# Kernel optimization log

Hardware: AMD Instinct MI355X
Metric: run time of the kernel (lower is better)

The kernel has to match this reference:

```python
import jax, jax.numpy as jnp
import numpy as np

B, L, HID, TRANS = 16384, 512, 768, 128


def setup_inputs() -> dict:
    key = jax.random.key(0)
    ks = jax.random.split(key, 12)
    def lin(k, out_d, in_d):
        kw, kb = jax.random.split(k)
        s = 1.0 / np.sqrt(in_d)
        return (jax.random.uniform(kw, (out_d, in_d), jnp.float32, -s, s),
                jax.random.uniform(kb, (out_d,), jnp.float32, -s, s))
    W_text, b_text = lin(ks[0], TRANS, HID)
    W_label, b_label = lin(ks[1], TRANS, HID)
    W0, b0 = lin(ks[2], TRANS, 2 * TRANS)
    W1, b1 = lin(ks[3], TRANS, TRANS)
    W2, b2 = lin(ks[4], 1, TRANS)
    target = jax.random.randint(ks[5], (B, L), 0, 2, jnp.int32)
    # guarantee every sample has at least one positive label (torch.mean on empty would NaN)
    target = target.at[:, 0].set(1)
    return {
        "text_embed": jax.random.normal(ks[6], (B, HID), jnp.float32),
        "label_embed": jax.random.normal(ks[7], (L, HID), jnp.float32),
        "target": target,
        "perm": jax.random.permutation(ks[8], B).astype(jnp.int32),
        "W_text": W_text, "b_text": b_text,
        "W_label": W_label, "b_label": b_label,
        "W0": W0, "b0": b0, "W1": W1, "b1": b1, "W2": W2, "b2": b2,
    }


def _network(t, l, W_text, b_text, W_label, b_label, W0, b0, W1, b1, W2, b2):
    tt = t @ W_text.T + b_text            # [B, trans]
    ll = l @ W_label.T + b_label          # [B, trans]
    h = jnp.concatenate([tt, ll], axis=1)  # [B, 2*trans]
    h = jax.nn.relu(h @ W0.T + b0)
    h = jax.nn.relu(h @ W1.T + b1)
    return h @ W2.T + b2                  # [B, 1]


def reference(text_embed, label_embed, target, perm,
              W_text, b_text, W_label, b_label, W0, b0, W1, b1, W2, b2):
    # variable-length mean pooling of label embeddings selected by the multi-hot target
    mask = target.astype(text_embed.dtype)                 # [B, L]
    counts = jnp.maximum(mask.sum(axis=1, keepdims=True), 1.0)
    label_feature_y = (mask @ label_embed) / counts        # [B, hid]
    negative_text = text_embed[perm]                       # shuffled negatives
    params = (W_text, b_text, W_label, b_label, W0, b0, W1, b1, W2, b2)
    E_joint = -jnp.mean(jax.nn.softplus(-_network(text_embed, label_feature_y, *params)))
    E_marginal = jnp.mean(jax.nn.softplus(_network(negative_text, label_feature_y, *params)))
    return E_marginal - E_joint
```

## Files before the change

### kernel.cpp

```cpp
#include <hip/hip_runtime.h>
#include <math.h>

#define BATCH 16384
#define LBL   512
#define HID   768
#define TR    128

typedef unsigned long long u64;
typedef unsigned short ushort_t;
typedef __attribute__((ext_vector_type(8))) short short8;
typedef __attribute__((ext_vector_type(4))) float f32x4;

__device__ __forceinline__ ushort_t f2bf(float f){
  unsigned u = __builtin_bit_cast(unsigned, f);
  u += 0x7FFFu + ((u >> 16) & 1u);
  return (ushort_t)(u >> 16);
}
__device__ __forceinline__ float bf2f(ushort_t h){
  unsigned u = ((unsigned)h) << 16;
  return __builtin_bit_cast(float, u);
}
__device__ __forceinline__ float softplusf(float x){
  return fmaxf(x, 0.0f) + log1pf(expf(-fabsf(x)));
}
__device__ __forceinline__ void gload_lds16(const void* g, void* l){
  __builtin_amdgcn_global_load_lds((const __attribute__((address_space(1))) void*)g,
                                   (__attribute__((address_space(3))) void*)l, 16, 0, 0);
}

__global__ __launch_bounds__(256) void k1(
    const float* __restrict__ W0, const float* __restrict__ Wt, const float* __restrict__ Wl,
    const float* __restrict__ bt, const float* __restrict__ bl, const float* __restrict__ b0,
    const float* __restrict__ W1,
    ushort_t* __restrict__ Msw, ushort_t* __restrict__ Qsw, ushort_t* __restrict__ W1B,
    float* __restrict__ KV, float* __restrict__ out){
  __shared__ float sw[TR];
  int bi = blockIdx.x, t = threadIdx.x;
  if (bi < 256){
    int i = bi & 127;
    int isQ = bi >> 7;
    const float* src = isQ ? Wl : Wt;
    ushort_t* dst = isQ ? Qsw : Msw;
    if (t < TR) sw[t] = W0[(size_t)i*256 + isQ*128 + t];
    if (!isQ && t < 128) W1B[i*128 + t] = f2bf(W1[i*128 + t]);
    __syncthreads();
    int c = t;
    float a0 = 0.f, a1 = 0.f, a2 = 0.f;
    #pragma unroll 8
    for (int a = 0; a < 128; a++){
      float w = sw[a];
      const float* r = src + (size_t)a*HID;
      a0 = fmaf(w, r[c], a0);
      a1 = fmaf(w, r[c+256], a1);
      a2 = fmaf(w, r[c+512], a2);
    }
    int c7 = c & 7;
    dst[(((c      )>>3)<<10) + (i<<3) + c7] = f2bf(a0);
    dst[(((c + 256)>>3)<<10) + (i<<3) + c7] = f2bf(a1);
    dst[(((c + 512)>>3)<<10) + (i<<3) + c7] = f2bf(a2);
  } else {
    if (t < TR){
      float s = b0[t];
      const float* r = W0 + (size_t)t*256;
      for (int a = 0; a < 128; a++) s = fmaf(r[a], bt[a], s);
      for (int a = 0; a < 128; a++) s = fmaf(r[128+a], bl[a], s);
      KV[t] = s;
    }
    if (t == 0) out[0] = 0.f;
  }
}

__device__ __forceinline__ void gemm768_32(const float* ap, const ushort_t* Bsw,
                                           ushort_t* As_, ushort_t* Bs_,
                                           int tid, int wave, int m, int q,
                                           f32x4 acc[2][2]){
  float4 ra0 = *(const float4*)ap;
  float4 ra1 = *(const float4*)(ap + 4);
  {
    const char* gb = (const char*)Bsw;
    char* lb = (char*)Bs_;
    #pragma unroll
    for (int p = 0; p < 4; p++)
      gload_lds16(gb + p*4096 + tid*16, lb + p*4096 + tid*16);
  }
  #pragma unroll
  for (int rt = 0; rt < 2; rt++)
    #pragma unroll
    for (int ct = 0; ct < 2; ct++)
      acc[rt][ct] = (f32x4){0.f,0.f,0.f,0.f};

  for (int c = 0; c < 12; c++){
    int buf = c & 1;
    short8 av;
    av[0] = (short)f2bf(ra0.x); av[1] = (short)f2bf(ra0.y);
    av[2] = (short)f2bf(ra0.z); av[3] = (short)f2bf(ra0.w);
    av[4] = (short)f2bf(ra1.x); av[5] = (short)f2bf(ra1.y);
    av[6] = (short)f2bf(ra1.z); av[7] = (short)f2bf(ra1.w);
    *(short8*)(As_ + (size_t)(buf*32 + (tid >> 3))*80 + (tid & 7)*8) = av;
    __syncthreads();
    if (c < 11){
      ra0 = *(const float4*)(ap + (c+1)*64);
      ra1 = *(const float4*)(ap + (c+1)*64 + 4);
      const char* gb = (const char*)Bsw + (size_t)(c+1)*16384;
      char* lb = (char*)(Bs_ + (buf^1)*8192);
      #pragma unroll
      for (int p = 0; p < 4; p++)
        gload_lds16(gb + p*4096 + tid*16, lb + p*4096 + tid*16);
    }
    #pragma unroll
    for (int kcc = 0; kcc < 2; kcc++){
      short8 bfr[2];
      #pragma unroll
      for (int ct = 0; ct < 2; ct++)
        bfr[ct] = *(const short8*)(Bs_ + buf*8192 + (kcc*4 + q)*1024 + (wave*32 + ct*16 + m)*8);
      #pragma unroll
      for (int rt = 0; rt < 2; rt++){
        short8 a = *(const short8*)(As_ + (size_t)(buf*32 + rt*16 + m)*80 + kcc*32 + q*8);
        #pragma unroll
        for (int ct = 0; ct < 2; ct++)
          acc[rt][ct] = __builtin_amdgcn_mfma_f32_16x16x32_bf16(a, bfr[ct], acc[rt][ct], 0, 0, 0);
      }
    }
  }
}

__global__ __launch_bounds__(256) void k2(
    const float* __restrict__ labe, const ushort_t* __restrict__ Qsw,
    const float* __restrict__ T,    const ushort_t* __restrict__ Msw,
    const float* __restrict__ KV,   const int* __restrict__ tgt,
    ushort_t* __restrict__ Gt, ushort_t* __restrict__ U,
    u64* __restrict__ bits, float* __restrict__ inv){
  __shared__ __align__(16) char uni[43008];
  int bi = blockIdx.x, tid = threadIdx.x;
  int lane = tid & 63, wave = tid >> 6;
  int m = lane & 15, q = lane >> 4;
  int arow = tid >> 3, ak = (tid & 7) * 8;
  ushort_t* Bs_ = (ushort_t*)uni;
  ushort_t* As_ = (ushort_t*)(uni + 32768);

  if (bi < 512){
    int b0r = bi*32;
    #pragma unroll
    for (int rr = 0; rr < 8; rr++){
      int row = b0r + wave*8 + rr;
      const int* rp = tgt + (size_t)row*LBL;
      int v[8];
      #pragma unroll
      for (int c = 0; c < 8; c++) v[c] = rp[c*64 + lane];
      int cnt = 0;
      #pragma unroll
      for (int c = 0; c < 8; c++){
        u64 mm = __ballot(v[c] != 0);
        if (lane == 0){ bits[(size_t)row*8 + c] = mm; cnt += __popcll(mm); }
      }
      if (lane == 0) inv[row] = 1.0f / (float)(cnt < 1 ? 1 : cnt);
    }
  } else if (bi < 528){
    int l0 = (bi - 512) * 32;
    f32x4 accG[2][2];
    gemm768_32(labe + (size_t)(l0 + arow)*HID + ak, Qsw, As_, Bs_, tid, wave, m, q, accG);
    __syncthreads();
    ushort_t (*GTs)[40] = (ushort_t(*)[40])uni;
    #pragma unroll
    for (int rt = 0; rt < 2; rt++)
      #pragma unroll
      for (int ct = 0; ct < 2; ct++){
        int col = wave*32 + ct*16 + m;
        #pragma unroll
        for (int r = 0; r < 4; r++)
          GTs[col][rt*16 + q*4 + r] = f2bf(accG[rt][ct][r]);
      }
    __syncthreads();
    int gi = tid >> 1, half = tid & 1;
    ushort_t* dstp = Gt + (size_t)gi*LBL + l0 + half*16;
    *(short8*)(dstp)     = *(const short8*)&GTs[gi][half*16];
    *(short8*)(dstp + 8) = *(const short8*)&GTs[gi][half*16 + 8];
  } else {
    int r0 = (bi - 528) * 32;
    f32x4 accU[2][2];
    gemm768_32(T + (size_t)(r0 + arow)*HID + ak, Msw, As_, Bs_, tid, wave, m, q, accU);
    #pragma unroll
    for (int rt = 0; rt < 2; rt++)
      #pragma unroll
      for (int ct = 0; ct < 2; ct++){
        int col = wave*32 + ct*16 + m;
        float kv = KV[col];
        #pragma unroll
        for (int r = 0; r < 4; r++)
          U[(size_t)(r0 + rt*16 + q*4 + r)*TR + col] = f2bf(accU[rt][ct][r] + kv);
      }
  }
}

__global__ __launch_bounds__(256) void k3(const ushort_t* __restrict__ U, const ushort_t* __restrict__ Gt,
                                          const u64* __restrict__ BITS_, const float* __restrict__ INV,
                                          const int* __restrict__ perm, const ushort_t* __restrict__ W1b,
                                          const float* __restrict__ b1, const float* __restrict__ W2,
                                          const float* __restrict__ b2, float* __restrict__ out){
  __shared__ __align__(16) u64 bitsS[32*10];
  __shared__ __align__(16) ushort_t h0s[64][136];
  __shared__ float sred[4*4*16*17];
  __shared__ float invs[32];
  __shared__ int   permS[32];

  int tid = threadIdx.x;
  int lane = tid & 63, wave = tid >> 6;
  int m = lane & 15, q = lane >> 4;
  int r0 = blockIdx.x * 32;

  if (tid < 128){
    int row = tid >> 2, seg = tid & 3;
    const int4* src = (const int4*)((const char*)BITS_ + (size_t)(r0+row)*64 + seg*16);
    *(int4*)((char*)bitsS + row*80 + seg*16) = *src;
  } else if (tid < 160){
    invs[tid & 31] = INV[r0 + (tid & 31)];
  } else if (tid < 192){
    permS[tid & 31] = perm[r0 + (tid & 31)];
  }
  __syncthreads();

  float up[2][2][4], un[2][2][4];
  #pragma unroll
  for (int rt = 0; rt < 2; rt++)
    #pragma unroll
    for (int ct = 0; ct < 2; ct++){
      int col = wave*32 + ct*16 + m;
      #pragma unroll
      for (int r = 0; r < 4; r++){
        int rowl = rt*16 + q*4 + r;
        up[rt][ct][r] = bf2f(U[(size_t)(r0 + rowl)*TR + col]);
        un[rt][ct][r] = bf2f(U[(size_t)permS[rowl]*TR + col]);
      }
    }

  const unsigned char* bits_b = (const unsigned char*)bitsS;
  f32x4 accV[2][2] = {{{0,0,0,0},{0,0,0,0}},{{0,0,0,0},{0,0,0,0}}};
  const ushort_t* gp[2];
  #pragma unroll
  for (int ct = 0; ct < 2; ct++)
    gp[ct] = Gt + (size_t)(wave*32 + ct*16 + m)*LBL + q*8;
  short8 bcur[2], bnext[2];
  #pragma unroll
  for (int ct = 0; ct < 2; ct++) bcur[ct] = *(const short8*)(gp[ct]);
  for (int c = 0; c < 16; c++){
    if (c < 15){
      #pragma unroll
      for (int ct = 0; ct < 2; ct++) bnext[ct] = *(const short8*)(gp[ct] + (c+1)*32);
    }
    #pragma unroll
    for (int rt = 0; rt < 2; rt++){
      unsigned bb = bits_b[(rt*16 + m)*80 + c*4 + q];
      short8 a;
      #pragma unroll
      for (int j = 0; j < 8; j++) a[j] = (short)(((bb >> j) & 1u) ? 0x3F80 : 0);
      #pragma unroll
      for (int ct = 0; ct < 2; ct++)
        accV[rt][ct] = __builtin_amdgcn_mfma_f32_16x16x32_bf16(a, bcur[ct], accV[rt][ct], 0, 0, 0);
    }
    #pragma unroll
    for (int ct = 0; ct < 2; ct++) bcur[ct] = bnext[ct];
  }

  #pragma unroll
  for (int rt = 0; rt < 2; rt++)
    #pragma unroll
    for (int ct = 0; ct < 2; ct++){
      int col = wave*32 + ct*16 + m;
      #pragma unroll
      for (int r = 0; r < 4; r++){
        int rowl = rt*16 + q*4 + r;
        float v = accV[rt][ct][r] * invs[rowl];
        h0s[rowl][col]      = f2bf(fmaxf(up[rt][ct][r] + v, 0.f));
        h0s[32 + rowl][col] = f2bf(fmaxf(un[rt][ct][r] + v, 0.f));
      }
    }
  __syncthreads();

  float w2c[2], b1c[2];
  #pragma unroll
  for (int ct = 0; ct < 2; ct++){
    int col = wave*32 + ct*16 + m;
    w2c[ct] = W2[col];
    b1c[ct] = b1[col];
  }
  float b2v = b2[0];

  #pragma unroll
  for (int rt2 = 0; rt2 < 4; rt2++){
    f32x4 accH[2] = {{0,0,0,0},{0,0,0,0}};
    #pragma unroll
    for (int kc = 0; kc < 4; kc++){
      short8 a = *(const short8*)&h0s[rt2*16 + m][kc*32 + q*8];
      #pragma unroll
      for (int ct = 0; ct < 2; ct++){
        short8 b = *(const short8*)(W1b + (size_t)(wave*32 + ct*16 + m)*TR + kc*32 + q*8);
        accH[ct] = __builtin_amdgcn_mfma_f32_16x16x32_bf16(a, b, accH[ct], 0, 0, 0);
      }
    }
    #pragma unroll
    for (int r = 0; r < 4; r++){
      float sp = 0.f;
      #pragma unroll
      for (int ct = 0; ct < 2; ct++)
        sp = fmaf(w2c[ct], fmaxf(accH[ct][r] + b1c[ct], 0.f), sp);
      sred[((wave*4 + rt2)*16 + q*4 + r)*17 + m] = sp;
    }
  }
  __syncthreads();

  if (tid < 64){
    int rt2 = tid >> 4, row = tid & 15;
    float s = b2v;
    #pragma unroll
    for (int wx = 0; wx < 4; wx++)
      #pragma unroll
      for (int n = 0; n < 16; n++) s += sred[((wx*4 + rt2)*16 + row)*17 + n];
    float val = (rt2 < 2) ? softplusf(-s) : softplusf(s);
    #pragma unroll
    for (int off = 32; off > 0; off >>= 1) val += __shfl_down(val, off);
    if (tid == 0) atomicAdd(out, val * (1.0f / (float)BATCH));
  }
}

extern "C" void kernel_launch(void* const* d_in, const int* in_sizes, int n_in,
                              void* d_out, int out_size, void* d_ws, size_t ws_size,
                              hipStream_t stream){
  const float* text = (const float*)d_in[0];
  const float* labe = (const float*)d_in[1];
  const int*   tgt  = (const int*)  d_in[2];
  const int*   perm = (const int*)  d_in[3];
  const float* Wt   = (const float*)d_in[4];
  const float* bt   = (const float*)d_in[5];
  const float* Wl   = (const float*)d_in[6];
  const float* bl   = (const float*)d_in[7];
  const float* W0   = (const float*)d_in[8];
  const float* b0   = (const float*)d_in[9];
  const float* W1   = (const float*)d_in[10];
  const float* b1   = (const float*)d_in[11];
  const float* W2   = (const float*)d_in[12];
  const float* b2   = (const float*)d_in[13];

  char* wsb = (char*)d_ws;
  size_t off = 0;
  auto alloc = [&](size_t bytes){
    size_t r = off;
    off += (bytes + 255) & ~(size_t)255;
    return r;
  };
  ushort_t* MSW = (ushort_t*)(wsb + alloc((size_t)TR*HID*2));
  ushort_t* QSW = (ushort_t*)(wsb + alloc((size_t)TR*HID*2));
  ushort_t* GT  = (ushort_t*)(wsb + alloc((size_t)TR*LBL*2));
  ushort_t* W1B = (ushort_t*)(wsb + alloc((size_t)TR*TR*2));
  float*    KV  = (float*)   (wsb + alloc((size_t)TR*4));
  u64*      BITS= (u64*)     (wsb + alloc((size_t)BATCH*8*8));
  float*    INV = (float*)   (wsb + alloc((size_t)BATCH*4));
  ushort_t* U   = (ushort_t*)(wsb + alloc((size_t)BATCH*TR*2));
  float*    out = (float*)d_out;
  (void)ws_size; (void)in_sizes; (void)n_in; (void)out_size;

  k1<<<257, 256, 0, stream>>>(W0, Wt, Wl, bt, bl, b0, W1, MSW, QSW, W1B, KV, out);
  k2<<<1040, 256, 0, stream>>>(labe, QSW, text, MSW, KV, tgt, GT, U, BITS, INV);
  k3<<<512, 256, 0, stream>>>(U, GT, BITS, INV, perm, W1B, b1, W2, b2, out);
}
```

Before: 175.8 us.

## Fuse text projection GEMM into final kernel, computing permuted negatives directly

The text-side GEMM (T @ Msw + KV) moves out of k2 into k3. Each block computes the projection for its own 32 rows and for the 32 permuted negative rows straight from text_embed, so the bf16 U intermediate and its gather are no longer needed. This removes a global write and read of the U buffer and shrinks k2's grid. The cost is that permuted text rows are projected a second time (double GEMM FLOPs for the text part) and k3 now uses more LDS and registers.

```diff
diff --git a/kernel.cpp b/kernel.cpp
--- a/kernel.cpp
+++ b/kernel.cpp
@@ -15,10 +15,6 @@
   unsigned u = __builtin_bit_cast(unsigned, f);
   u += 0x7FFFu + ((u >> 16) & 1u);
   return (ushort_t)(u >> 16);
-}
-__device__ __forceinline__ float bf2f(ushort_t h){
-  unsigned u = ((unsigned)h) << 16;
-  return __builtin_bit_cast(float, u);
 }
 __device__ __forceinline__ float softplusf(float x){
   return fmaxf(x, 0.0f) + log1pf(expf(-fabsf(x)));
@@ -126,37 +122,18 @@
 
 __global__ __launch_bounds__(256) void k2(
     const float* __restrict__ labe, const ushort_t* __restrict__ Qsw,
-    const float* __restrict__ T,    const ushort_t* __restrict__ Msw,
-    const float* __restrict__ KV,   const int* __restrict__ tgt,
-    ushort_t* __restrict__ Gt, ushort_t* __restrict__ U,
-    u64* __restrict__ bits, float* __restrict__ inv){
+    const int* __restrict__ tgt,
+    ushort_t* __restrict__ Gt, u64* __restrict__ bits, float* __restrict__ inv){
   __shared__ __align__(16) char uni[43008];
   int bi = blockIdx.x, tid = threadIdx.x;
   int lane = tid & 63, wave = tid >> 6;
   int m = lane & 15, q = lane >> 4;
-  int arow = tid >> 3, ak = (tid & 7) * 8;
   ushort_t* Bs_ = (ushort_t*)uni;
   ushort_t* As_ = (ushort_t*)(uni + 32768);
 
-  if (bi < 512){
-    int b0r = bi*32;
-    #pragma unroll
-    for (int rr = 0; rr < 8; rr++){
-      int row = b0r + wave*8 + rr;
-      const int* rp = tgt + (size_t)row*LBL;
-      int v[8];
-      #pragma unroll
-      for (int c = 0; c < 8; c++) v[c] = rp[c*64 + lane];
-      int cnt = 0;
-      #pragma unroll
-      for (int c = 0; c < 8; c++){
-        u64 mm = __ballot(v[c] != 0);
-        if (lane == 0){ bits[(size_t)row*8 + c] = mm; cnt += __popcll(mm); }
-      }
-      if (lane == 0) inv[row] = 1.0f / (float)(cnt < 1 ? 1 : cnt);
-    }
-  } else if (bi < 528){
-    int l0 = (bi - 512) * 32;
+  if (bi < 16){
+    int l0 = bi * 32;
+    int arow = tid >> 3, ak = (tid & 7) * 8;
     f32x4 accG[2][2];
     gemm768_32(labe + (size_t)(l0 + arow)*HID + ak, Qsw, As_, Bs_, tid, wave, m, q, accG);
     __syncthreads();
@@ -176,37 +153,41 @@
     *(short8*)(dstp)     = *(const short8*)&GTs[gi][half*16];
     *(short8*)(dstp + 8) = *(const short8*)&GTs[gi][half*16 + 8];
   } else {
-    int r0 = (bi - 528) * 32;
-    f32x4 accU[2][2];
-    gemm768_32(T + (size_t)(r0 + arow)*HID + ak, Msw, As_, Bs_, tid, wave, m, q, accU);
-    #pragma unroll
-    for (int rt = 0; rt < 2; rt++)
-      #pragma unroll
-      for (int ct = 0; ct < 2; ct++){
-        int col = wave*32 + ct*16 + m;
-        float kv = KV[col];
-        #pragma unroll
-        for (int r = 0; r < 4; r++)
-          U[(size_t)(r0 + rt*16 + q*4 + r)*TR + col] = f2bf(accU[rt][ct][r] + kv);
-      }
-  }
-}
-
-__global__ __launch_bounds__(256) void k3(const ushort_t* __restrict__ U, const ushort_t* __restrict__ Gt,
+    int b0r = (bi - 16)*32;
+    #pragma unroll
+    for (int rr = 0; rr < 8; rr++){
+      int row = b0r + wave*8 + rr;
+      const int* rp = tgt + (size_t)row*LBL;
+      int v[8];
+      #pragma unroll
+      for (int c = 0; c < 8; c++) v[c] = rp[c*64 + lane];
+      int cnt = 0;
+      #pragma unroll
+      for (int c = 0; c < 8; c++){
+        u64 mm = __ballot(v[c] != 0);
+        if (lane == 0){ bits[(size_t)row*8 + c] = mm; cnt += __popcll(mm); }
+      }
+      if (lane == 0) inv[row] = 1.0f / (float)(cnt < 1 ? 1 : cnt);
+    }
+  }
+}
+
+__global__ __launch_bounds__(256) void k3(const float* __restrict__ T, const ushort_t* __restrict__ Msw,
+                                          const float* __restrict__ KV, const ushort_t* __restrict__ Gt,
                                           const u64* __restrict__ BITS_, const float* __restrict__ INV,
                                           const int* __restrict__ perm, const ushort_t* __restrict__ W1b,
                                           const float* __restrict__ b1, const float* __restrict__ W2,
                                           const float* __restrict__ b2, float* __restrict__ out){
+  __shared__ __align__(16) char uni[51200];
   __shared__ __align__(16) u64 bitsS[32*10];
-  __shared__ __align__(16) ushort_t h0s[64][136];
-  __shared__ float sred[4*4*16*17];
   __shared__ float invs[32];
-  __shared__ int   permS[32];
 
   int tid = threadIdx.x;
   int lane = tid & 63, wave = tid >> 6;
   int m = lane & 15, q = lane >> 4;
   int r0 = blockIdx.x * 32;
+  ushort_t* Bs_ = (ushort_t*)uni;
+  ushort_t* As_ = (ushort_t*)(uni + 32768);
 
   if (tid < 128){
     int row = tid >> 2, seg = tid & 3;
@@ -214,24 +195,67 @@
     *(int4*)((char*)bitsS + row*80 + seg*16) = *src;
   } else if (tid < 160){
     invs[tid & 31] = INV[r0 + (tid & 31)];
-  } else if (tid < 192){
-    permS[tid & 31] = perm[r0 + (tid & 31)];
-  }
-  __syncthreads();
-
-  float up[2][2][4], un[2][2][4];
-  #pragma unroll
-  for (int rt = 0; rt < 2; rt++)
-    #pragma unroll
-    for (int ct = 0; ct < 2; ct++){
-      int col = wave*32 + ct*16 + m;
-      #pragma unroll
-      for (int r = 0; r < 4; r++){
-        int rowl = rt*16 + q*4 + r;
-        up[rt][ct][r] = bf2f(U[(size_t)(r0 + rowl)*TR + col]);
-        un[rt][ct][r] = bf2f(U[(size_t)permS[rowl]*TR + col]);
-      }
-    }
+  }
+
+  int ar = tid >> 3, ak = (tid & 7) * 8;
+  const float* app = T + (size_t)(r0 + ar)*HID + ak;
+  int pg = perm[r0 + ar];
+  const float* apn = T + (size_t)pg*HID + ak;
+
+  float4 pa0 = *(const float4*)(app);
+  float4 pa1 = *(const float4*)(app + 4);
+  float4 na0 = *(const float4*)(apn);
+  float4 na1 = *(const float4*)(apn + 4);
+  {
+    const char* gb = (const char*)Msw;
+    char* lb = (char*)Bs_;
+    #pragma unroll
+    for (int p = 0; p < 4; p++)
+      gload_lds16(gb + p*4096 + tid*16, lb + p*4096 + tid*16);
+  }
+  f32x4 acc[4][2];
+  #pragma unroll
+  for (int rt = 0; rt < 4; rt++)
+    #pragma unroll
+    for (int ct = 0; ct < 2; ct++)
+      acc[rt][ct] = (f32x4){0.f,0.f,0.f,0.f};
+
+  for (int c = 0; c < 12; c++){
+    int buf = c & 1;
+    short8 pv, nv;
+    pv[0]=(short)f2bf(pa0.x); pv[1]=(short)f2bf(pa0.y); pv[2]=(short)f2bf(pa0.z); pv[3]=(short)f2bf(pa0.w);
+    pv[4]=(short)f2bf(pa1.x); pv[5]=(short)f2bf(pa1.y); pv[6]=(short)f2bf(pa1.z); pv[7]=(short)f2bf(pa1.w);
+    nv[0]=(short)f2bf(na0.x); nv[1]=(short)f2bf(na0.y); nv[2]=(short)f2bf(na0.z); nv[3]=(short)f2bf(na0.w);
+    nv[4]=(short)f2bf(na1.x); nv[5]=(short)f2bf(na1.y); nv[6]=(short)f2bf(na1.z); nv[7]=(short)f2bf(na1.w);
+    *(short8*)(As_ + (size_t)(buf*64 + ar)*72 + ak)      = pv;
+    *(short8*)(As_ + (size_t)(buf*64 + 32 + ar)*72 + ak) = nv;
+    __syncthreads();
+    if (c < 11){
+      pa0 = *(const float4*)(app + (c+1)*64);
+      pa1 = *(const float4*)(app + (c+1)*64 + 4);
+      na0 = *(const float4*)(apn + (c+1)*64);
+      na1 = *(const float4*)(apn + (c+1)*64 + 4);
+      const char* gb = (const char*)Msw + (size_t)(c+1)*16384;
+      char* lb = (char*)(Bs_ + (buf^1)*8192);
+      #pragma unroll
+      for (int p = 0; p < 4; p++)
+        gload_lds16(gb + p*4096 + tid*16, lb + p*4096 + tid*16);
+    }
+    #pragma unroll
+    for (int kcc = 0; kcc < 2; kcc++){
+      short8 bfr[2];
+      #pragma unroll
+      for (int ct = 0; ct < 2; ct++)
+        bfr[ct] = *(const short8*)(Bs_ + buf*8192 + (kcc*4 + q)*1024 + (wave*32 + ct*16 + m)*8);
+      #pragma unroll
+      for (int rt = 0; rt < 4; rt++){
+        short8 a = *(const short8*)(As_ + (size_t)(buf*64 + rt*16 + m)*72 + kcc*32 + q*8);
+        #pragma unroll
+        for (int ct = 0; ct < 2; ct++)
+          acc[rt][ct] = __builtin_amdgcn_mfma_f32_16x16x32_bf16(a, bfr[ct], acc[rt][ct], 0, 0, 0);
+      }
+    }
+  }
 
   const unsigned char* bits_b = (const unsigned char*)bitsS;
   f32x4 accV[2][2] = {{{0,0,0,0},{0,0,0,0}},{{0,0,0,0},{0,0,0,0}}};
@@ -261,17 +285,21 @@
     for (int ct = 0; ct < 2; ct++) bcur[ct] = bnext[ct];
   }
 
+  __syncthreads();
+  ushort_t (*h0s)[136] = (ushort_t(*)[136])uni;
+  float* sred = (float*)(uni + 17408);
   #pragma unroll
   for (int rt = 0; rt < 2; rt++)
     #pragma unroll
     for (int ct = 0; ct < 2; ct++){
       int col = wave*32 + ct*16 + m;
+      float kv = KV[col];
       #pragma unroll
       for (int r = 0; r < 4; r++){
         int rowl = rt*16 + q*4 + r;
-        float v = accV[rt][ct][r] * invs[rowl];
-        h0s[rowl][col]      = f2bf(fmaxf(up[rt][ct][r] + v, 0.f));
-        h0s[32 + rowl][col] = f2bf(fmaxf(un[rt][ct][r] + v, 0.f));
+        float v = accV[rt][ct][r] * invs[rowl] + kv;
+        h0s[rowl][col]      = f2bf(fmaxf(acc[rt][ct][r]   + v, 0.f));
+        h0s[32 + rowl][col] = f2bf(fmaxf(acc[rt+2][ct][r] + v, 0.f));
       }
     }
   __syncthreads();
@@ -354,11 +382,10 @@
   float*    KV  = (float*)   (wsb + alloc((size_t)TR*4));
   u64*      BITS= (u64*)     (wsb + alloc((size_t)BATCH*8*8));
   float*    INV = (float*)   (wsb + alloc((size_t)BATCH*4));
-  ushort_t* U   = (ushort_t*)(wsb + alloc((size_t)BATCH*TR*2));
   float*    out = (float*)d_out;
   (void)ws_size; (void)in_sizes; (void)n_in; (void)out_size;
 
   k1<<<257, 256, 0, stream>>>(W0, Wt, Wl, bt, bl, b0, W1, MSW, QSW, W1B, KV, out);
-  k2<<<1040, 256, 0, stream>>>(labe, QSW, text, MSW, KV, tgt, GT, U, BITS, INV);
-  k3<<<512, 256, 0, stream>>>(U, GT, BITS, INV, perm, W1B, b1, W2, b2, out);
-}
+  k2<<<528, 256, 0, stream>>>(labe, QSW, tgt, GT, BITS, INV);
+  k3<<<512, 256, 0, stream>>>(text, MSW, KV, GT, BITS, INV, perm, W1B, b1, W2, b2, out);
+}
```

Result: faster. 171.6 us (-2.3%).

## Fuse text projection GEMM into final kernel, computing shuffled rows directly

Applied to the files above, without the earlier changes.

The text-embedding projection (T·M) moves out of k2 into k3, so the intermediate U buffer is no longer written and re-read. Each k3 block now computes the projection for its own 32 rows and for their 32 permuted negative rows. The GEMM drops the LDS staging and swizzled layout and reads fp32 A and row-major bf16 B straight from global memory into MFMA registers. This doubles the text GEMM work, since every row is projected once as a positive and once as a negative, and the operand loads are strided and uncoalesced.

```diff
diff --git a/kernel.cpp b/kernel.cpp
--- a/kernel.cpp
+++ b/kernel.cpp
@@ -16,23 +16,21 @@
   u += 0x7FFFu + ((u >> 16) & 1u);
   return (ushort_t)(u >> 16);
 }
-__device__ __forceinline__ float bf2f(ushort_t h){
-  unsigned u = ((unsigned)h) << 16;
-  return __builtin_bit_cast(float, u);
-}
 __device__ __forceinline__ float softplusf(float x){
   return fmaxf(x, 0.0f) + log1pf(expf(-fabsf(x)));
 }
-__device__ __forceinline__ void gload_lds16(const void* g, void* l){
-  __builtin_amdgcn_global_load_lds((const __attribute__((address_space(1))) void*)g,
-                                   (__attribute__((address_space(3))) void*)l, 16, 0, 0);
+__device__ __forceinline__ short8 cvt8(float4 x0, float4 x1){
+  short8 a;
+  a[0]=(short)f2bf(x0.x); a[1]=(short)f2bf(x0.y); a[2]=(short)f2bf(x0.z); a[3]=(short)f2bf(x0.w);
+  a[4]=(short)f2bf(x1.x); a[5]=(short)f2bf(x1.y); a[6]=(short)f2bf(x1.z); a[7]=(short)f2bf(x1.w);
+  return a;
 }
 
 __global__ __launch_bounds__(256) void k1(
     const float* __restrict__ W0, const float* __restrict__ Wt, const float* __restrict__ Wl,
     const float* __restrict__ bt, const float* __restrict__ bl, const float* __restrict__ b0,
     const float* __restrict__ W1,
-    ushort_t* __restrict__ Msw, ushort_t* __restrict__ Qsw, ushort_t* __restrict__ W1B,
+    ushort_t* __restrict__ Mbf, ushort_t* __restrict__ Qbf, ushort_t* __restrict__ W1B,
     float* __restrict__ KV, float* __restrict__ out){
   __shared__ float sw[TR];
   int bi = blockIdx.x, t = threadIdx.x;
@@ -40,7 +38,7 @@
     int i = bi & 127;
     int isQ = bi >> 7;
     const float* src = isQ ? Wl : Wt;
-    ushort_t* dst = isQ ? Qsw : Msw;
+    ushort_t* dst = isQ ? Qbf : Mbf;
     if (t < TR) sw[t] = W0[(size_t)i*256 + isQ*128 + t];
     if (!isQ && t < 128) W1B[i*128 + t] = f2bf(W1[i*128 + t]);
     __syncthreads();
@@ -54,10 +52,9 @@
       a1 = fmaf(w, r[c+256], a1);
       a2 = fmaf(w, r[c+512], a2);
     }
-    int c7 = c & 7;
-    dst[(((c      )>>3)<<10) + (i<<3) + c7] = f2bf(a0);
-    dst[(((c + 256)>>3)<<10) + (i<<3) + c7] = f2bf(a1);
-    dst[(((c + 512)>>3)<<10) + (i<<3) + c7] = f2bf(a2);
+    dst[(size_t)i*HID + c]       = f2bf(a0);
+    dst[(size_t)i*HID + c + 256] = f2bf(a1);
+    dst[(size_t)i*HID + c + 512] = f2bf(a2);
   } else {
     if (t < TR){
       float s = b0[t];
@@ -70,97 +67,42 @@
   }
 }
 
-__device__ __forceinline__ void gemm768_32(const float* ap, const ushort_t* Bsw,
-                                           ushort_t* As_, ushort_t* Bs_,
-                                           int tid, int wave, int m, int q,
-                                           f32x4 acc[2][2]){
-  float4 ra0 = *(const float4*)ap;
-  float4 ra1 = *(const float4*)(ap + 4);
-  {
-    const char* gb = (const char*)Bsw;
-    char* lb = (char*)Bs_;
-    #pragma unroll
-    for (int p = 0; p < 4; p++)
-      gload_lds16(gb + p*4096 + tid*16, lb + p*4096 + tid*16);
-  }
-  #pragma unroll
-  for (int rt = 0; rt < 2; rt++)
+__global__ __launch_bounds__(256) void k2(
+    const float* __restrict__ labe, const ushort_t* __restrict__ Qbf,
+    const int* __restrict__ tgt,
+    ushort_t* __restrict__ Gt, u64* __restrict__ bits, float* __restrict__ inv){
+  __shared__ __align__(16) ushort_t GTs[128][40];
+  int bi = blockIdx.x, tid = threadIdx.x;
+  int lane = tid & 63, wave = tid >> 6;
+  int m = lane & 15, q = lane >> 4;
+
+  if (bi < 16){
+    int l0 = bi * 32;
+    const float* ar[2];
+    ar[0] = labe + (size_t)(l0 + m)*HID + q*8;
+    ar[1] = labe + (size_t)(l0 + 16 + m)*HID + q*8;
+    const ushort_t* br[2];
     #pragma unroll
     for (int ct = 0; ct < 2; ct++)
-      acc[rt][ct] = (f32x4){0.f,0.f,0.f,0.f};
-
-  for (int c = 0; c < 12; c++){
-    int buf = c & 1;
-    short8 av;
-    av[0] = (short)f2bf(ra0.x); av[1] = (short)f2bf(ra0.y);
-    av[2] = (short)f2bf(ra0.z); av[3] = (short)f2bf(ra0.w);
-    av[4] = (short)f2bf(ra1.x); av[5] = (short)f2bf(ra1.y);
-    av[6] = (short)f2bf(ra1.z); av[7] = (short)f2bf(ra1.w);
-    *(short8*)(As_ + (size_t)(buf*32 + (tid >> 3))*80 + (tid & 7)*8) = av;
-    __syncthreads();
-    if (c < 11){
-      ra0 = *(const float4*)(ap + (c+1)*64);
-      ra1 = *(const float4*)(ap + (c+1)*64 + 4);
-      const char* gb = (const char*)Bsw + (size_t)(c+1)*16384;
-      char* lb = (char*)(Bs_ + (buf^1)*8192);
-      #pragma unroll
-      for (int p = 0; p < 4; p++)
-        gload_lds16(gb + p*4096 + tid*16, lb + p*4096 + tid*16);
-    }
-    #pragma unroll
-    for (int kcc = 0; kcc < 2; kcc++){
+      br[ct] = Qbf + (size_t)(wave*32 + ct*16 + m)*HID + q*8;
+
+    f32x4 acc[2][2] = {{{0,0,0,0},{0,0,0,0}},{{0,0,0,0},{0,0,0,0}}};
+    #pragma unroll 2
+    for (int c = 0; c < 24; c++){
       short8 bfr[2];
       #pragma unroll
       for (int ct = 0; ct < 2; ct++)
-        bfr[ct] = *(const short8*)(Bs_ + buf*8192 + (kcc*4 + q)*1024 + (wave*32 + ct*16 + m)*8);
+        bfr[ct] = *(const short8*)(br[ct] + c*32);
       #pragma unroll
       for (int rt = 0; rt < 2; rt++){
-        short8 a = *(const short8*)(As_ + (size_t)(buf*32 + rt*16 + m)*80 + kcc*32 + q*8);
+        float4 x0 = *(const float4*)(ar[rt] + c*32);
+        float4 x1 = *(const float4*)(ar[rt] + c*32 + 4);
+        short8 a = cvt8(x0, x1);
         #pragma unroll
         for (int ct = 0; ct < 2; ct++)
           acc[rt][ct] = __builtin_amdgcn_mfma_f32_16x16x32_bf16(a, bfr[ct], acc[rt][ct], 0, 0, 0);
       }
     }
-  }
-}
-
-__global__ __launch_bounds__(256) void k2(
-    const float* __restrict__ labe, const ushort_t* __restrict__ Qsw,
-    const float* __restrict__ T,    const ushort_t* __restrict__ Msw,
-    const float* __restrict__ KV,   const int* __restrict__ tgt,
-    ushort_t* __restrict__ Gt, ushort_t* __restrict__ U,
-    u64* __restrict__ bits, float* __restrict__ inv){
-  __shared__ __align__(16) char uni[43008];
-  int bi = blockIdx.x, tid = threadIdx.x;
-  int lane = tid & 63, wave = tid >> 6;
-  int m = lane & 15, q = lane >> 4;
-  int arow = tid >> 3, ak = (tid & 7) * 8;
-  ushort_t* Bs_ = (ushort_t*)uni;
-  ushort_t* As_ = (ushort_t*)(uni + 32768);
-
-  if (bi < 512){
-    int b0r = bi*32;
-    #pragma unroll
-    for (int rr = 0; rr < 8; rr++){
-      int row = b0r + wave*8 + rr;
-      const int* rp = tgt + (size_t)row*LBL;
-      int v[8];
-      #pragma unroll
-      for (int c = 0; c < 8; c++) v[c] = rp[c*64 + lane];
-      int cnt = 0;
-      #pragma unroll
-      for (int c = 0; c < 8; c++){
-        u64 mm = __ballot(v[c] != 0);
-        if (lane == 0){ bits[(size_t)row*8 + c] = mm; cnt += __popcll(mm); }
-      }
-      if (lane == 0) inv[row] = 1.0f / (float)(cnt < 1 ? 1 : cnt);
-    }
-  } else if (bi < 528){
-    int l0 = (bi - 512) * 32;
-    f32x4 accG[2][2];
-    gemm768_32(labe + (size_t)(l0 + arow)*HID + ak, Qsw, As_, Bs_, tid, wave, m, q, accG);
-    __syncthreads();
-    ushort_t (*GTs)[40] = (ushort_t(*)[40])uni;
     #pragma unroll
     for (int rt = 0; rt < 2; rt++)
       #pragma unroll
@@ -168,7 +110,7 @@
         int col = wave*32 + ct*16 + m;
         #pragma unroll
         for (int r = 0; r < 4; r++)
-          GTs[col][rt*16 + q*4 + r] = f2bf(accG[rt][ct][r]);
+          GTs[col][rt*16 + q*4 + r] = f2bf(acc[rt][ct][r]);
       }
     __syncthreads();
     int gi = tid >> 1, half = tid & 1;
@@ -176,23 +118,27 @@
     *(short8*)(dstp)     = *(const short8*)&GTs[gi][half*16];
     *(short8*)(dstp + 8) = *(const short8*)&GTs[gi][half*16 + 8];
   } else {
-    int r0 = (bi - 528) * 32;
-    f32x4 accU[2][2];
-    gemm768_32(T + (size_t)(r0 + arow)*HID + ak, Msw, As_, Bs_, tid, wave, m, q, accU);
-    #pragma unroll
-    for (int rt = 0; rt < 2; rt++)
-      #pragma unroll
-      for (int ct = 0; ct < 2; ct++){
-        int col = wave*32 + ct*16 + m;
-        float kv = KV[col];
-        #pragma unroll
-        for (int r = 0; r < 4; r++)
-          U[(size_t)(r0 + rt*16 + q*4 + r)*TR + col] = f2bf(accU[rt][ct][r] + kv);
-      }
-  }
-}
-
-__global__ __launch_bounds__(256) void k3(const ushort_t* __restrict__ U, const ushort_t* __restrict__ Gt,
+    int b0r = (bi - 16)*32;
+    #pragma unroll
+    for (int rr = 0; rr < 8; rr++){
+      int row = b0r + wave*8 + rr;
+      const int* rp = tgt + (size_t)row*LBL;
+      int v[8];
+      #pragma unroll
+      for (int c = 0; c < 8; c++) v[c] = rp[c*64 + lane];
+      int cnt = 0;
+      #pragma unroll
+      for (int c = 0; c < 8; c++){
+        u64 mm = __ballot(v[c] != 0);
+        if (lane == 0){ bits[(size_t)row*8 + c] = mm; cnt += __popcll(mm); }
+      }
+      if (lane == 0) inv[row] = 1.0f / (float)(cnt < 1 ? 1 : cnt);
+    }
+  }
+}
+
+__global__ __launch_bounds__(256) void k3(const float* __restrict__ T, const ushort_t* __restrict__ Mbf,
+                                          const float* __restrict__ KV, const ushort_t* __restrict__ Gt,
                                           const u64* __restrict__ BITS_, const float* __restrict__ INV,
                                           const int* __restrict__ perm, const ushort_t* __restrict__ W1b,
                                           const float* __restrict__ b1, const float* __restrict__ W2,
@@ -219,19 +165,39 @@
   }
   __syncthreads();
 
-  float up[2][2][4], un[2][2][4];
-  #pragma unroll
-  for (int rt = 0; rt < 2; rt++)
-    #pragma unroll
-    for (int ct = 0; ct < 2; ct++){
-      int col = wave*32 + ct*16 + m;
-      #pragma unroll
-      for (int r = 0; r < 4; r++){
-        int rowl = rt*16 + q*4 + r;
-        up[rt][ct][r] = bf2f(U[(size_t)(r0 + rowl)*TR + col]);
-        un[rt][ct][r] = bf2f(U[(size_t)permS[rowl]*TR + col]);
-      }
-    }
+  const float* ar[4];
+  ar[0] = T + (size_t)(r0 + m)*HID + q*8;
+  ar[1] = T + (size_t)(r0 + 16 + m)*HID + q*8;
+  ar[2] = T + (size_t)permS[m]*HID + q*8;
+  ar[3] = T + (size_t)permS[16 + m]*HID + q*8;
+  const ushort_t* br[2];
+  #pragma unroll
+  for (int ct = 0; ct < 2; ct++)
+    br[ct] = Mbf + (size_t)(wave*32 + ct*16 + m)*HID + q*8;
+
+  f32x4 acc[4][2];
+  #pragma unroll
+  for (int rt = 0; rt < 4; rt++)
+    #pragma unroll
+    for (int ct = 0; ct < 2; ct++)
+      acc[rt][ct] = (f32x4){0.f,0.f,0.f,0.f};
+
+  #pragma unroll 2
+  for (int c = 0; c < 24; c++){
+    short8 bfr[2];
+    #pragma unroll
+    for (int ct = 0; ct < 2; ct++)
+      bfr[ct] = *(const short8*)(br[ct] + c*32);
+    #pragma unroll
+    for (int rt = 0; rt < 4; rt++){
+      float4 x0 = *(const float4*)(ar[rt] + c*32);
+      float4 x1 = *(const float4*)(ar[rt] + c*32 + 4);
+      short8 a = cvt8(x0, x1);
+      #pragma unroll
+      for (int ct = 0; ct < 2; ct++)
+        acc[rt][ct] = __builtin_amdgcn_mfma_f32_16x16x32_bf16(a, bfr[ct], acc[rt][ct], 0, 0, 0);
+    }
+  }
 
   const unsigned char* bits_b = (const unsigned char*)bitsS;
   f32x4 accV[2][2] = {{{0,0,0,0},{0,0,0,0}},{{0,0,0,0},{0,0,0,0}}};
@@ -266,12 +232,13 @@
     #pragma unroll
     for (int ct = 0; ct < 2; ct++){
       int col = wave*32 + ct*16 + m;
+      float kv = KV[col];
       #pragma unroll
       for (int r = 0; r < 4; r++){
         int rowl = rt*16 + q*4 + r;
-        float v = accV[rt][ct][r] * invs[rowl];
-        h0s[rowl][col]      = f2bf(fmaxf(up[rt][ct][r] + v, 0.f));
-        h0s[32 + rowl][col] = f2bf(fmaxf(un[rt][ct][r] + v, 0.f));
+        float v = accV[rt][ct][r] * invs[rowl] + kv;
+        h0s[rowl][col]      = f2bf(fmaxf(acc[rt][ct][r]   + v, 0.f));
+        h0s[32 + rowl][col] = f2bf(fmaxf(acc[rt+2][ct][r] + v, 0.f));
       }
     }
   __syncthreads();
@@ -347,18 +314,17 @@
     off += (bytes + 255) & ~(size_t)255;
     return r;
   };
-  ushort_t* MSW = (ushort_t*)(wsb + alloc((size_t)TR*HID*2));
-  ushort_t* QSW = (ushort_t*)(wsb + alloc((size_t)TR*HID*2));
+  ushort_t* MBF = (ushort_t*)(wsb + alloc((size_t)TR*HID*2));
+  ushort_t* QBF = (ushort_t*)(wsb + alloc((size_t)TR*HID*2));
   ushort_t* GT  = (ushort_t*)(wsb + alloc((size_t)TR*LBL*2));
   ushort_t* W1B = (ushort_t*)(wsb + alloc((size_t)TR*TR*2));
   float*    KV  = (float*)   (wsb + alloc((size_t)TR*4));
   u64*      BITS= (u64*)     (wsb + alloc((size_t)BATCH*8*8));
   float*    INV = (float*)   (wsb + alloc((size_t)BATCH*4));
-  ushort_t* U   = (ushort_t*)(wsb + alloc((size_t)BATCH*TR*2));
   float*    out = (float*)d_out;
   (void)ws_size; (void)in_sizes; (void)n_in; (void)out_size;
 
-  k1<<<257, 256, 0, stream>>>(W0, Wt, Wl, bt, bl, b0, W1, MSW, QSW, W1B, KV, out);
-  k2<<<1040, 256, 0, stream>>>(labe, QSW, text, MSW, KV, tgt, GT, U, BITS, INV);
-  k3<<<512, 256, 0, stream>>>(U, GT, BITS, INV, perm, W1B, b1, W2, b2, out);
-}
+  k1<<<257, 256, 0, stream>>>(W0, Wt, Wl, bt, bl, b0, W1, MBF, QBF, W1B, KV, out);
+  k2<<<528, 256, 0, stream>>>(labe, QBF, tgt, GT, BITS, INV);
+  k3<<<512, 256, 0, stream>>>(text, MBF, KV, GT, BITS, INV, perm, W1B, b1, W2, b2, out);
+}
```

Measured after the change: 216.8 us. 23.3% more time.
